# Optimization experiments

Measured on AMD Instinct MI355X. Metric: run time of the kernel, lower is better.

## Reference

```python
import jax, jax.numpy as jnp
import numpy as np

B = 4096
N_DENSE = 13
N_SPARSE = 26
VOCAB = 100000
EMB = 8
CIN_SIZE = [26, 128, 128]


def setup_inputs() -> dict:
    key = jax.random.key(0)
    ks = jax.random.split(key, 24)
    s = 0.05
    dense = jax.random.normal(ks[0], (B, N_DENSE), dtype=jnp.float32)
    sparse = jax.random.randint(ks[1], (B, N_SPARSE), 0, VOCAB).astype(jnp.float32)
    inputs = jnp.concatenate([dense, sparse], axis=1)  # [B, 39]
    emb_tables = jax.random.normal(ks[2], (N_SPARSE, VOCAB, EMB), dtype=jnp.float32) * s
    linear_W = jax.random.normal(ks[3], (39, 1), dtype=jnp.float32) * s
    linear_b = jnp.zeros((1,), dtype=jnp.float32)
    # CIN Conv3d weights: kernel (H_prev, H0, 1) with out_channels H_next -> [H_next, H_prev, H0]
    W_cin0 = jax.random.normal(ks[4], (CIN_SIZE[1], CIN_SIZE[0], CIN_SIZE[0]), dtype=jnp.float32) * s
    b_cin0 = jnp.zeros((CIN_SIZE[1],), dtype=jnp.float32)
    W_cin1 = jax.random.normal(ks[5], (CIN_SIZE[2], CIN_SIZE[1], CIN_SIZE[0]), dtype=jnp.float32) * s
    b_cin1 = jnp.zeros((CIN_SIZE[2],), dtype=jnp.float32)
    cin_lin_W = jax.random.normal(ks[6], (256, 1), dtype=jnp.float32) * s
    cin_lin_b = jnp.zeros((1,), dtype=jnp.float32)
    d_W1 = jax.random.normal(ks[7], (221, 256), dtype=jnp.float32) * s
    d_b1 = jnp.zeros((256,), dtype=jnp.float32)
    d_W2 = jax.random.normal(ks[8], (256, 128), dtype=jnp.float32) * s
    d_b2 = jnp.zeros((128,), dtype=jnp.float32)
    d_W3 = jax.random.normal(ks[9], (128, 64), dtype=jnp.float32) * s
    d_b3 = jnp.zeros((64,), dtype=jnp.float32)
    d_W4 = jax.random.normal(ks[10], (64, 1), dtype=jnp.float32) * s
    d_b4 = jnp.zeros((1,), dtype=jnp.float32)
    return dict(inputs=inputs, emb_tables=emb_tables, linear_W=linear_W, linear_b=linear_b,
                W_cin0=W_cin0, b_cin0=b_cin0, W_cin1=W_cin1, b_cin1=b_cin1,
                cin_lin_W=cin_lin_W, cin_lin_b=cin_lin_b,
                d_W1=d_W1, d_b1=d_b1, d_W2=d_W2, d_b2=d_b2,
                d_W3=d_W3, d_b3=d_b3, d_W4=d_W4, d_b4=d_b4)


def reference(inputs, emb_tables, linear_W, linear_b,
              W_cin0, b_cin0, W_cin1, b_cin1, cin_lin_W, cin_lin_b,
              d_W1, d_b1, d_W2, d_b2, d_W3, d_b3, d_W4, d_b4):
    dense_in = inputs[:, :N_DENSE]                       # [B, 13]
    sparse_idx = inputs[:, N_DENSE:].astype(jnp.int32)   # [B, 26]

    # linear part over the raw inputs
    linear_out = inputs @ linear_W + linear_b            # [B, 1]

    # per-field embedding lookup: tables [F, V, E], idx [B, F] -> emb [B, F, E]
    emb = jax.vmap(lambda t, i: t[i], in_axes=(0, 1), out_axes=1)(emb_tables, sparse_idx)

    # CIN: each layer is an outer product over fields followed by a full-extent
    # Conv3d, i.e. X_{l+1}[b,o,k] = sum_{i,j} X_l[b,i,k] * X_0[b,j,k] * W[o,i,j] + b[o]
    X0 = emb
    Xi = emb
    res = []
    for W, b in ((W_cin0, b_cin0), (W_cin1, b_cin1)):
        Xi = jnp.einsum('bik,bjk,oij->bok', Xi, X0, W) + b[None, :, None]
        res.append(Xi)
    cin_feat = jnp.sum(jnp.concatenate(res, axis=1), axis=-1)  # [B, 256]
    cin_out = jax.nn.relu(cin_feat @ cin_lin_W + cin_lin_b)    # [B, 1]

    # dense MLP over [dense | flattened embeddings]
    h = jnp.concatenate([dense_in, emb.reshape(emb.shape[0], -1)], axis=1)  # [B, 221]
    h = jax.nn.relu(h @ d_W1 + d_b1)
    h = jax.nn.relu(h @ d_W2 + d_b2)
    h = jax.nn.relu(h @ d_W3 + d_b3)
    dense_out = jax.nn.relu(h @ d_W4 + d_b4)                   # [B, 1]

    return jax.nn.sigmoid(linear_out + cin_out + dense_out).reshape(-1)  # [B]
```

## Files before the change

### kernel.cpp

```cpp
#include <hip/hip_runtime.h>
#include <math.h>

#define B     4096
#define ND    13
#define NS    26
#define NF    39
#define VOCAB 100000
#define NP    351
#define NPP   360
#define CHP   45
#define GSTR  28
#define RPB   8
#define TPB   512
#define XSS   212

#define OFF_GST 0
#define OFF_CST 10080
#define OFF_C2J 10088

__global__ __launch_bounds__(256) void k_pre(const float* __restrict__ W0,
                                             const float* __restrict__ W1,
                                             const float* __restrict__ b0,
                                             const float* __restrict__ b1,
                                             const float* __restrict__ clw,
                                             float* __restrict__ Gst,
                                             float* __restrict__ cst,
                                             float* __restrict__ c2j) {
    int blk = blockIdx.x, tid = threadIdx.x;
    if (blk < 26) {
        int j = blk;
        __shared__ float vh[2][128];
        __shared__ float vj[128];
        __shared__ float c2r[2];
        {
            int i = tid & 127, h = tid >> 7;
            const float* wp = W1 + (long)(h * 64) * 3328 + i * 26 + j;
            float acc = 0.f;
#pragma unroll 8
            for (int o = 0; o < 64; o++) acc += clw[128 + h * 64 + o] * wp[o * 3328];
            vh[h][i] = acc;
        }
        __syncthreads();
        if (tid < 128) {
            float vv = vh[0][tid] + vh[1][tid];
            vj[tid] = vv;
            float c = vv * b0[tid];
            for (int off = 32; off; off >>= 1) c += __shfl_down(c, off, 64);
            if ((tid & 63) == 0) c2r[tid >> 6] = c;
        }
        __syncthreads();
        if (tid == 0) c2j[j] = c2r[0] + c2r[1];
        for (int p = tid; p < NPP; p += 256) {
            float g = 0.f;
            if (p < NP) {
                int l = 0, rem = p;
                while (rem >= NS - l) { rem -= NS - l; l++; }
                int m = l + rem;
                float sym = (l != m) ? 1.f : 0.f;
                const float* wa = W0 + l * 26 + m;
                const float* wb = W0 + m * 26 + l;
#pragma unroll 8
                for (int i = 0; i < 128; i++)
                    g += vj[i] * (wa[i * 676] + sym * wb[i * 676]);
            }
            Gst[p * GSTR + j] = g;
        }
    } else if (blk == 26) {
        for (int p = tid; p < NPP; p += 256) {
            float a = 0.f; int lmbits = 0;
            if (p < NP) {
                int l = 0, rem = p;
                while (rem >= NS - l) { rem -= NS - l; l++; }
                int m = l + rem;
                float sym = (l != m) ? 1.f : 0.f;
                const float* wa = W0 + l * 26 + m;
                const float* wb = W0 + m * 26 + l;
#pragma unroll 8
                for (int o = 0; o < 128; o++)
                    a += clw[o] * (wa[o * 676] + sym * wb[o * 676]);
                lmbits = (l << 5) | m;
            }
            Gst[p * GSTR + 26] = a;
            Gst[p * GSTR + 27] = __int_as_float(lmbits);
        }
    } else {
        __shared__ float red[2];
        float c = 0.f;
        if (tid < 128) {
            c = clw[tid] * b0[tid] + clw[128 + tid] * b1[tid];
            for (int off = 32; off; off >>= 1) c += __shfl_down(c, off, 64);
            if ((tid & 63) == 0) red[tid >> 6] = c;
        }
        __syncthreads();
        if (tid == 0) cst[0] = 8.f * (red[0] + red[1]);
    }
}

__global__ __launch_bounds__(512, 4) void k_main(
    const float* __restrict__ inputs, const float* __restrict__ tables,
    const float* __restrict__ lW, const float* __restrict__ lb,
    const float* __restrict__ Gst, const float* __restrict__ c2j,
    const float* __restrict__ cst,
    const float* __restrict__ dW1, const float* __restrict__ db1,
    const float* __restrict__ dW2, const float* __restrict__ db2,
    const float* __restrict__ dW3, const float* __restrict__ db3,
    const float* __restrict__ dW4, const float* __restrict__ db4,
    const float* __restrict__ clb,
    float* __restrict__ out) {
    __shared__ float insf[RPB][40];
    __shared__ float xs[RPB][XSS];
    __shared__ float4 inT4[448];
    __shared__ float h1Tf[256 * 12];
    __shared__ float4 pbuf4[1024];
    __shared__ float lin_s[RPB], scin_s[RPB];
    __shared__ float redbuf[8][RPB];

    float* inTf = (float*)inT4;
    float* h2Tf = (float*)inT4;

    int tid = threadIdx.x;
    int b0r = blockIdx.x * RPB;

    if (tid < RPB * NS) {
        int r = tid / NS, f = tid - r * NS;
        float fidx = inputs[(b0r + r) * NF + ND + f];
        int idx = (int)fidx;
        const float4* src = (const float4*)(tables + ((long)f * VOCAB + idx) * 8);
        float4 a = src[0], b4 = src[1];
        *(float4*)&xs[r][f * 8] = a;
        *(float4*)&xs[r][f * 8 + 4] = b4;
    }
    for (int e = tid; e < RPB * NF; e += TPB) {
        int r = e / NF, c = e - r * NF;
        insf[r][c] = inputs[(b0r + r) * NF + c];
    }
    if (tid >= 496 && tid < 496 + RPB) {
        int r = tid - 496;
        float acc = lb[0];
        for (int c = 0; c < NF; c++) acc += inputs[(b0r + r) * NF + c] * lW[c];
        lin_s[r] = acc;
    }
    __syncthreads();

    for (int e = tid; e < 221 * RPB; e += TPB) {
        int c = e >> 3, r = e & 7;
        inTf[c * 8 + r] = (c < ND) ? insf[r][c] : xs[r][c - ND];
    }
    {
        int w = tid >> 6;
        int wu = __builtin_amdgcn_readfirstlane(w);
        int lane = tid & 63;
        int row = lane >> 3, k = lane & 7;
        const float4* g4 = (const float4*)Gst + wu * CHP * 7;
        const float* xrow = &xs[row][0];
        float csel = (wu == 0) ? 1.f : 0.f;
        float t[27];
#pragma unroll
        for (int j = 0; j < 27; j++) t[j] = 0.f;
#pragma unroll 3
        for (int pi = 0; pi < CHP; pi++) {
            float4 g6 = g4[pi * 7 + 6];
            int lm = __float_as_int(g6.w);
            float q = xrow[(lm >> 5) * 8 + k] * xrow[(lm & 31) * 8 + k];
            float4 g0 = g4[pi * 7 + 0], g1 = g4[pi * 7 + 1];
            float4 g2 = g4[pi * 7 + 2], g3 = g4[pi * 7 + 3];
            float4 g4v = g4[pi * 7 + 4], g5 = g4[pi * 7 + 5];
            t[0]  += g0.x * q; t[1]  += g0.y * q; t[2]  += g0.z * q; t[3]  += g0.w * q;
            t[4]  += g1.x * q; t[5]  += g1.y * q; t[6]  += g1.z * q; t[7]  += g1.w * q;
            t[8]  += g2.x * q; t[9]  += g2.y * q; t[10] += g2.z * q; t[11] += g2.w * q;
            t[12] += g3.x * q; t[13] += g3.y * q; t[14] += g3.z * q; t[15] += g3.w * q;
            t[16] += g4v.x * q; t[17] += g4v.y * q; t[18] += g4v.z * q; t[19] += g4v.w * q;
            t[20] += g5.x * q; t[21] += g5.y * q; t[22] += g5.z * q; t[23] += g5.w * q;
            t[24] += g6.x * q; t[25] += g6.y * q; t[26] += g6.z * q;
        }
        float part = t[26];
#pragma unroll
        for (int j = 0; j < 26; j++) {
            float xv = xrow[j * 8 + k];
            part += (t[j] + csel * c2j[j]) * xv;
        }
        part += __shfl_xor(part, 1, 64);
        part += __shfl_xor(part, 2, 64);
        part += __shfl_xor(part, 4, 64);
        if (k == 0) redbuf[w][row] = part;
    }
    __syncthreads();

    {
        int p = tid & 127, h = (tid >> 7) & 1, cg = tid >> 8;
        int c0 = cg ? 111 : 0;
        int c1 = cg ? 221 : 111;
        float4 A0 = make_float4(0.f, 0.f, 0.f, 0.f);
        float4 A1 = A0;
#pragma unroll 4
        for (int c = c0; c < c1; c++) {
            float2 wv = *(const float2*)&dW1[c * 256 + 2 * p];
            float4 iv = *(const float4*)&inTf[c * 8 + 4 * h];
            A0.x += iv.x * wv.x; A0.y += iv.y * wv.x; A0.z += iv.z * wv.x; A0.w += iv.w * wv.x;
            A1.x += iv.x * wv.y; A1.y += iv.y * wv.y; A1.z += iv.z * wv.y; A1.w += iv.w * wv.y;
        }
        pbuf4[tid * 2]     = A0;
        pbuf4[tid * 2 + 1] = A1;
    }
    __syncthreads();

    if (tid < 256) {
        int o = tid;
        float bb = db1[o];
        float4 a0 = pbuf4[o],       b0v = pbuf4[512 + o];
        float4 a1 = pbuf4[256 + o], b1v = pbuf4[768 + o];
        float4 S0, S1;
        S0.x = fmaxf(a0.x + b0v.x + bb, 0.f); S0.y = fmaxf(a0.y + b0v.y + bb, 0.f);
        S0.z = fmaxf(a0.z + b0v.z + bb, 0.f); S0.w = fmaxf(a0.w + b0v.w + bb, 0.f);
        S1.x = fmaxf(a1.x + b1v.x + bb, 0.f); S1.y = fmaxf(a1.y + b1v.y + bb, 0.f);
        S1.z = fmaxf(a1.z + b1v.z + bb, 0.f); S1.w = fmaxf(a1.w + b1v.w + bb, 0.f);
        *(float4*)&h1Tf[o * 12]     = S0;
        *(float4*)&h1Tf[o * 12 + 4] = S1;
    }
    if (tid >= 256 && tid < 256 + RPB) {
        int r = tid - 256;
        float s = cst[0];
#pragma unroll
        for (int w = 0; w < 8; w++) s += redbuf[w][r];
        scin_s[r] = s;
    }
    __syncthreads();

    {
        int p = tid & 63, h = (tid >> 6) & 1, cg = tid >> 7;
        int c0 = cg << 6;
        float4 A0 = make_float4(0.f, 0.f, 0.f, 0.f);
        float4 A1 = A0;
#pragma unroll 4
        for (int cc = 0; cc < 64; cc++) {
            int c = c0 + cc;
            float2 wv = *(const float2*)&dW2[c * 128 + 2 * p];
            float4 iv = *(const float4*)&h1Tf[c * 12 + 4 * h];
            A0.x += iv.x * wv.x; A0.y += iv.y * wv.x; A0.z += iv.z * wv.x; A0.w += iv.w * wv.x;
            A1.x += iv.x * wv.y; A1.y += iv.y * wv.y; A1.z += iv.z * wv.y; A1.w += iv.w * wv.y;
        }
        pbuf4[tid * 2]     = A0;
        pbuf4[tid * 2 + 1] = A1;
    }
    __syncthreads();

    if (tid < 128) {
        int o = tid;
        float bb = db2[o];
        float sx0 = bb, sy0 = bb, sz0 = bb, sw0 = bb;
        float sx1 = bb, sy1 = bb, sz1 = bb, sw1 = bb;
#pragma unroll
        for (int cg = 0; cg < 4; cg++) {
            float4 p0 = pbuf4[cg * 256 + o];
            float4 p1 = pbuf4[cg * 256 + 128 + o];
            sx0 += p0.x; sy0 += p0.y; sz0 += p0.z; sw0 += p0.w;
            sx1 += p1.x; sy1 += p1.y; sz1 += p1.z; sw1 += p1.w;
        }
        float4 S0, S1;
        S0.x = fmaxf(sx0, 0.f); S0.y = fmaxf(sy0, 0.f);
        S0.z = fmaxf(sz0, 0.f); S0.w = fmaxf(sw0, 0.f);
        S1.x = fmaxf(sx1, 0.f); S1.y = fmaxf(sy1, 0.f);
        S1.z = fmaxf(sz1, 0.f); S1.w = fmaxf(sw1, 0.f);
        *(float4*)&h2Tf[o * 12]     = S0;
        *(float4*)&h2Tf[o * 12 + 4] = S1;
    }
    __syncthreads();

    {
        int cg = tid >> 6, lane = tid & 63;
        int p = lane & 31, h = lane >> 5;
        int c0 = cg << 4;
        float4 A0 = make_float4(0.f, 0.f, 0.f, 0.f);
        float4 A1 = A0;
#pragma unroll 8
        for (int cc = 0; cc < 16; cc++) {
            int c = c0 + cc;
            float2 wv = *(const float2*)&dW3[c * 64 + 2 * p];
            float4 iv = *(const float4*)&h2Tf[c * 12 + 4 * h];
            A0.x += iv.x * wv.x; A0.y += iv.y * wv.x; A0.z += iv.z * wv.x; A0.w += iv.w * wv.x;
            A1.x += iv.x * wv.y; A1.y += iv.y * wv.y; A1.z += iv.z * wv.y; A1.w += iv.w * wv.y;
        }
        pbuf4[tid * 2]     = A0;
        pbuf4[tid * 2 + 1] = A1;
    }
    __syncthreads();

    if (tid < 64) {
        int o = tid;
        float4 S0 = make_float4(0.f, 0.f, 0.f, 0.f);
        float4 S1 = S0;
#pragma unroll
        for (int cg = 0; cg < 8; cg++) {
            float4 p0 = pbuf4[cg * 128 + o];
            float4 p1 = pbuf4[cg * 128 + 64 + o];
            S0.x += p0.x; S0.y += p0.y; S0.z += p0.z; S0.w += p0.w;
            S1.x += p1.x; S1.y += p1.y; S1.z += p1.z; S1.w += p1.w;
        }
        float b3 = db3[o], w4 = dW4[o];
        S0.x = fmaxf(S0.x + b3, 0.f) * w4; S0.y = fmaxf(S0.y + b3, 0.f) * w4;
        S0.z = fmaxf(S0.z + b3, 0.f) * w4; S0.w = fmaxf(S0.w + b3, 0.f) * w4;
        S1.x = fmaxf(S1.x + b3, 0.f) * w4; S1.y = fmaxf(S1.y + b3, 0.f) * w4;
        S1.z = fmaxf(S1.z + b3, 0.f) * w4; S1.w = fmaxf(S1.w + b3, 0.f) * w4;
#pragma unroll
        for (int off = 1; off < 64; off <<= 1) {
            S0.x += __shfl_xor(S0.x, off, 64); S0.y += __shfl_xor(S0.y, off, 64);
            S0.z += __shfl_xor(S0.z, off, 64); S0.w += __shfl_xor(S0.w, off, 64);
            S1.x += __shfl_xor(S1.x, off, 64); S1.y += __shfl_xor(S1.y, off, 64);
            S1.z += __shfl_xor(S1.z, off, 64); S1.w += __shfl_xor(S1.w, off, 64);
        }
        if (tid == 0) {
            float sv[8] = { S0.x, S0.y, S0.z, S0.w, S1.x, S1.y, S1.z, S1.w };
            float bb = db4[0], cb = clb[0];
#pragma unroll
            for (int r = 0; r < RPB; r++) {
                float dense = fmaxf(sv[r] + bb, 0.f);
                float cin = fmaxf(scin_s[r] + cb, 0.f);
                float x = lin_s[r] + cin + dense;
                out[b0r + r] = 1.f / (1.f + expf(-x));
            }
        }
    }
}

extern "C" void kernel_launch(void* const* d_in, const int* in_sizes, int n_in,
                              void* d_out, int out_size, void* d_ws, size_t ws_size,
                              hipStream_t stream) {
    const float* inputs = (const float*)d_in[0];
    const float* tables = (const float*)d_in[1];
    const float* lW     = (const float*)d_in[2];
    const float* lb     = (const float*)d_in[3];
    const float* W0     = (const float*)d_in[4];
    const float* b0     = (const float*)d_in[5];
    const float* W1c    = (const float*)d_in[6];
    const float* b1c    = (const float*)d_in[7];
    const float* clw    = (const float*)d_in[8];
    const float* clb    = (const float*)d_in[9];
    const float* dW1    = (const float*)d_in[10];
    const float* db1    = (const float*)d_in[11];
    const float* dW2    = (const float*)d_in[12];
    const float* db2    = (const float*)d_in[13];
    const float* dW3    = (const float*)d_in[14];
    const float* db3    = (const float*)d_in[15];
    const float* dW4    = (const float*)d_in[16];
    const float* db4    = (const float*)d_in[17];

    float* ws   = (float*)d_ws;
    float* Gst  = ws + OFF_GST;
    float* cst  = ws + OFF_CST;
    float* c2j  = ws + OFF_C2J;

    k_pre<<<28, 256, 0, stream>>>(W0, W1c, b0, b1c, clw, Gst, cst, c2j);
    k_main<<<B / RPB, TPB, 0, stream>>>(inputs, tables, lW, lb, Gst, c2j, cst,
                                        dW1, db1, dW2, db2, dW3, db3, dW4, db4, clb,
                                        (float*)d_out);
}
```

Before: 208.9 us.

## Overlap CIN and first dense layer across warp halves, drop partial reductions

Splits the block so four warps compute the CIN quadratic form, each handling two chunks, while the other four warps compute the full first MLP layer over all 221 inputs without a split-K partial buffer. Other changes: the embedding gather now uses two threads per field, (l,m) index pairs come from a separate LUT, MLP layers 2 and 3 use one output per thread, and the final reduction is spread across all warps. The aim is to remove several barriers and partial-sum passes and to let CIN and dense work run concurrently. The cost is fewer threads per stage and more serial work per thread in each half, which may lengthen the critical path.

```diff
diff --git a/kernel.cpp b/kernel.cpp
--- a/kernel.cpp
+++ b/kernel.cpp
@@ -17,6 +17,7 @@
 #define OFF_GST 0
 #define OFF_CST 10080
 #define OFF_C2J 10088
+#define OFF_LUT 10120
 
 __global__ __launch_bounds__(256) void k_pre(const float* __restrict__ W0,
                                              const float* __restrict__ W1,
@@ -25,7 +26,8 @@
                                              const float* __restrict__ clw,
                                              float* __restrict__ Gst,
                                              float* __restrict__ cst,
-                                             float* __restrict__ c2j) {
+                                             float* __restrict__ c2j,
+                                             int* __restrict__ lutg) {
     int blk = blockIdx.x, tid = threadIdx.x;
     if (blk < 26) {
         int j = blk;
@@ -82,6 +84,7 @@
             }
             Gst[p * GSTR + 26] = a;
             Gst[p * GSTR + 27] = __int_as_float(lmbits);
+            lutg[p] = lmbits;
         }
     } else {
         __shared__ float red[2];
@@ -100,147 +103,130 @@
     const float* __restrict__ inputs, const float* __restrict__ tables,
     const float* __restrict__ lW, const float* __restrict__ lb,
     const float* __restrict__ Gst, const float* __restrict__ c2j,
-    const float* __restrict__ cst,
+    const float* __restrict__ cst, const int* __restrict__ lutg,
     const float* __restrict__ dW1, const float* __restrict__ db1,
     const float* __restrict__ dW2, const float* __restrict__ db2,
     const float* __restrict__ dW3, const float* __restrict__ db3,
     const float* __restrict__ dW4, const float* __restrict__ db4,
     const float* __restrict__ clb,
     float* __restrict__ out) {
-    __shared__ float insf[RPB][40];
     __shared__ float xs[RPB][XSS];
-    __shared__ float4 inT4[448];
+    __shared__ float inTf[221 * 8];
     __shared__ float h1Tf[256 * 12];
     __shared__ float4 pbuf4[1024];
-    __shared__ float lin_s[RPB], scin_s[RPB];
-    __shared__ float redbuf[8][RPB];
-
-    float* inTf = (float*)inT4;
-    float* h2Tf = (float*)inT4;
+    __shared__ float lin_s[RPB];
+    __shared__ float redbuf[4][RPB];
+
+    float* h2Tf = inTf;
+    float* pbufF = (float*)pbuf4;
 
     int tid = threadIdx.x;
     int b0r = blockIdx.x * RPB;
 
-    if (tid < RPB * NS) {
-        int r = tid / NS, f = tid - r * NS;
-        float fidx = inputs[(b0r + r) * NF + ND + f];
-        int idx = (int)fidx;
+    if (tid < 416) {
+        int r = tid / 52, t2 = tid - r * 52;
+        int f = t2 >> 1, hf = t2 & 1;
+        int idx = (int)inputs[(b0r + r) * NF + ND + f];
         const float4* src = (const float4*)(tables + ((long)f * VOCAB + idx) * 8);
-        float4 a = src[0], b4 = src[1];
-        *(float4*)&xs[r][f * 8] = a;
-        *(float4*)&xs[r][f * 8 + 4] = b4;
-    }
-    for (int e = tid; e < RPB * NF; e += TPB) {
-        int r = e / NF, c = e - r * NF;
-        insf[r][c] = inputs[(b0r + r) * NF + c];
-    }
-    if (tid >= 496 && tid < 496 + RPB) {
-        int r = tid - 496;
+        *(float4*)&xs[r][f * 8 + hf * 4] = src[hf];
+    }
+    if (tid >= 448 && tid < 448 + RPB) {
+        int r = tid - 448;
         float acc = lb[0];
         for (int c = 0; c < NF; c++) acc += inputs[(b0r + r) * NF + c] * lW[c];
         lin_s[r] = acc;
     }
     __syncthreads();
 
-    for (int e = tid; e < 221 * RPB; e += TPB) {
+    for (int e = tid; e < 221 * 8; e += TPB) {
         int c = e >> 3, r = e & 7;
-        inTf[c * 8 + r] = (c < ND) ? insf[r][c] : xs[r][c - ND];
-    }
+        inTf[c * 8 + r] = (c < ND) ? inputs[(b0r + r) * NF + c] : xs[r][c - ND];
+    }
+    __syncthreads();
+
     {
         int w = tid >> 6;
         int wu = __builtin_amdgcn_readfirstlane(w);
         int lane = tid & 63;
-        int row = lane >> 3, k = lane & 7;
-        const float4* g4 = (const float4*)Gst + wu * CHP * 7;
-        const float* xrow = &xs[row][0];
-        float csel = (wu == 0) ? 1.f : 0.f;
-        float t[27];
-#pragma unroll
-        for (int j = 0; j < 27; j++) t[j] = 0.f;
-#pragma unroll 3
-        for (int pi = 0; pi < CHP; pi++) {
-            float4 g6 = g4[pi * 7 + 6];
-            int lm = __float_as_int(g6.w);
-            float q = xrow[(lm >> 5) * 8 + k] * xrow[(lm & 31) * 8 + k];
-            float4 g0 = g4[pi * 7 + 0], g1 = g4[pi * 7 + 1];
-            float4 g2 = g4[pi * 7 + 2], g3 = g4[pi * 7 + 3];
-            float4 g4v = g4[pi * 7 + 4], g5 = g4[pi * 7 + 5];
-            t[0]  += g0.x * q; t[1]  += g0.y * q; t[2]  += g0.z * q; t[3]  += g0.w * q;
-            t[4]  += g1.x * q; t[5]  += g1.y * q; t[6]  += g1.z * q; t[7]  += g1.w * q;
-            t[8]  += g2.x * q; t[9]  += g2.y * q; t[10] += g2.z * q; t[11] += g2.w * q;
-            t[12] += g3.x * q; t[13] += g3.y * q; t[14] += g3.z * q; t[15] += g3.w * q;
-            t[16] += g4v.x * q; t[17] += g4v.y * q; t[18] += g4v.z * q; t[19] += g4v.w * q;
-            t[20] += g5.x * q; t[21] += g5.y * q; t[22] += g5.z * q; t[23] += g5.w * q;
-            t[24] += g6.x * q; t[25] += g6.y * q; t[26] += g6.z * q;
-        }
-        float part = t[26];
-#pragma unroll
-        for (int j = 0; j < 26; j++) {
-            float xv = xrow[j * 8 + k];
-            part += (t[j] + csel * c2j[j]) * xv;
-        }
-        part += __shfl_xor(part, 1, 64);
-        part += __shfl_xor(part, 2, 64);
-        part += __shfl_xor(part, 4, 64);
-        if (k == 0) redbuf[w][row] = part;
+        if (wu < 4) {
+            int row = lane >> 3, k = lane & 7;
+            const float* xrow = &xs[row][0];
+            float t[27];
+#pragma unroll
+            for (int j = 0; j < 27; j++) t[j] = 0.f;
+#pragma unroll 1
+            for (int half = 0; half < 2; half++) {
+                int ch = 2 * wu + half;
+                const float4* g4 = (const float4*)Gst + ch * CHP * 7;
+                const int* lu = lutg + ch * CHP;
+#pragma unroll 5
+                for (int pi = 0; pi < CHP; pi++) {
+                    int lm = lu[pi];
+                    float q = xrow[(lm >> 5) * 8 + k] * xrow[(lm & 31) * 8 + k];
+                    float4 g0 = g4[pi * 7 + 0], g1 = g4[pi * 7 + 1];
+                    float4 g2 = g4[pi * 7 + 2], g3 = g4[pi * 7 + 3];
+                    float4 g4v = g4[pi * 7 + 4], g5 = g4[pi * 7 + 5];
+                    float4 g6 = g4[pi * 7 + 6];
+                    t[0]  += g0.x * q; t[1]  += g0.y * q; t[2]  += g0.z * q; t[3]  += g0.w * q;
+                    t[4]  += g1.x * q; t[5]  += g1.y * q; t[6]  += g1.z * q; t[7]  += g1.w * q;
+                    t[8]  += g2.x * q; t[9]  += g2.y * q; t[10] += g2.z * q; t[11] += g2.w * q;
+                    t[12] += g3.x * q; t[13] += g3.y * q; t[14] += g3.z * q; t[15] += g3.w * q;
+                    t[16] += g4v.x * q; t[17] += g4v.y * q; t[18] += g4v.z * q; t[19] += g4v.w * q;
+                    t[20] += g5.x * q; t[21] += g5.y * q; t[22] += g5.z * q; t[23] += g5.w * q;
+                    t[24] += g6.x * q; t[25] += g6.y * q; t[26] += g6.z * q;
+                }
+            }
+            float csel = (wu == 0) ? 1.f : 0.f;
+            float part = t[26];
+#pragma unroll
+            for (int j = 0; j < 26; j++) {
+                float xv = xrow[j * 8 + k];
+                part += (t[j] + csel * c2j[j]) * xv;
+            }
+            part += __shfl_xor(part, 1, 64);
+            part += __shfl_xor(part, 2, 64);
+            part += __shfl_xor(part, 4, 64);
+            if (k == 0) redbuf[wu][row] = part;
+        } else {
+            int o = tid & 255;
+            float4 S0 = make_float4(0.f, 0.f, 0.f, 0.f);
+            float4 S1 = S0;
+#pragma unroll 4
+            for (int c = 0; c < 221; c++) {
+                float wv = dW1[c * 256 + o];
+                float4 i0 = *(const float4*)&inTf[c * 8];
+                float4 i1 = *(const float4*)&inTf[c * 8 + 4];
+                S0.x += i0.x * wv; S0.y += i0.y * wv; S0.z += i0.z * wv; S0.w += i0.w * wv;
+                S1.x += i1.x * wv; S1.y += i1.y * wv; S1.z += i1.z * wv; S1.w += i1.w * wv;
+            }
+            float bb = db1[o];
+            S0.x = fmaxf(S0.x + bb, 0.f); S0.y = fmaxf(S0.y + bb, 0.f);
+            S0.z = fmaxf(S0.z + bb, 0.f); S0.w = fmaxf(S0.w + bb, 0.f);
+            S1.x = fmaxf(S1.x + bb, 0.f); S1.y = fmaxf(S1.y + bb, 0.f);
+            S1.z = fmaxf(S1.z + bb, 0.f); S1.w = fmaxf(S1.w + bb, 0.f);
+            *(float4*)&h1Tf[o * 12]     = S0;
+            *(float4*)&h1Tf[o * 12 + 4] = S1;
+        }
     }
     __syncthreads();
 
     {
-        int p = tid & 127, h = (tid >> 7) & 1, cg = tid >> 8;
-        int c0 = cg ? 111 : 0;
-        int c1 = cg ? 221 : 111;
-        float4 A0 = make_float4(0.f, 0.f, 0.f, 0.f);
-        float4 A1 = A0;
-#pragma unroll 4
-        for (int c = c0; c < c1; c++) {
-            float2 wv = *(const float2*)&dW1[c * 256 + 2 * p];
-            float4 iv = *(const float4*)&inTf[c * 8 + 4 * h];
-            A0.x += iv.x * wv.x; A0.y += iv.y * wv.x; A0.z += iv.z * wv.x; A0.w += iv.w * wv.x;
-            A1.x += iv.x * wv.y; A1.y += iv.y * wv.y; A1.z += iv.z * wv.y; A1.w += iv.w * wv.y;
-        }
-        pbuf4[tid * 2]     = A0;
-        pbuf4[tid * 2 + 1] = A1;
-    }
-    __syncthreads();
-
-    if (tid < 256) {
-        int o = tid;
-        float bb = db1[o];
-        float4 a0 = pbuf4[o],       b0v = pbuf4[512 + o];
-        float4 a1 = pbuf4[256 + o], b1v = pbuf4[768 + o];
-        float4 S0, S1;
-        S0.x = fmaxf(a0.x + b0v.x + bb, 0.f); S0.y = fmaxf(a0.y + b0v.y + bb, 0.f);
-        S0.z = fmaxf(a0.z + b0v.z + bb, 0.f); S0.w = fmaxf(a0.w + b0v.w + bb, 0.f);
-        S1.x = fmaxf(a1.x + b1v.x + bb, 0.f); S1.y = fmaxf(a1.y + b1v.y + bb, 0.f);
-        S1.z = fmaxf(a1.z + b1v.z + bb, 0.f); S1.w = fmaxf(a1.w + b1v.w + bb, 0.f);
-        *(float4*)&h1Tf[o * 12]     = S0;
-        *(float4*)&h1Tf[o * 12 + 4] = S1;
-    }
-    if (tid >= 256 && tid < 256 + RPB) {
-        int r = tid - 256;
-        float s = cst[0];
-#pragma unroll
-        for (int w = 0; w < 8; w++) s += redbuf[w][r];
-        scin_s[r] = s;
-    }
-    __syncthreads();
-
-    {
-        int p = tid & 63, h = (tid >> 6) & 1, cg = tid >> 7;
+        int o = tid & 127, cg = tid >> 7;
         int c0 = cg << 6;
         float4 A0 = make_float4(0.f, 0.f, 0.f, 0.f);
         float4 A1 = A0;
 #pragma unroll 4
         for (int cc = 0; cc < 64; cc++) {
             int c = c0 + cc;
-            float2 wv = *(const float2*)&dW2[c * 128 + 2 * p];
-            float4 iv = *(const float4*)&h1Tf[c * 12 + 4 * h];
-            A0.x += iv.x * wv.x; A0.y += iv.y * wv.x; A0.z += iv.z * wv.x; A0.w += iv.w * wv.x;
-            A1.x += iv.x * wv.y; A1.y += iv.y * wv.y; A1.z += iv.z * wv.y; A1.w += iv.w * wv.y;
-        }
-        pbuf4[tid * 2]     = A0;
-        pbuf4[tid * 2 + 1] = A1;
+            float wv = dW2[c * 128 + o];
+            float4 i0 = *(const float4*)&h1Tf[c * 12];
+            float4 i1 = *(const float4*)&h1Tf[c * 12 + 4];
+            A0.x += i0.x * wv; A0.y += i0.y * wv; A0.z += i0.z * wv; A0.w += i0.w * wv;
+            A1.x += i1.x * wv; A1.y += i1.y * wv; A1.z += i1.z * wv; A1.w += i1.w * wv;
+        }
+        int pb = (cg * 128 + o) * 2;
+        pbuf4[pb]     = A0;
+        pbuf4[pb + 1] = A1;
     }
     __syncthreads();
 
@@ -251,8 +237,8 @@
         float sx1 = bb, sy1 = bb, sz1 = bb, sw1 = bb;
 #pragma unroll
         for (int cg = 0; cg < 4; cg++) {
-            float4 p0 = pbuf4[cg * 256 + o];
-            float4 p1 = pbuf4[cg * 256 + 128 + o];
+            float4 p0 = pbuf4[(cg * 128 + o) * 2];
+            float4 p1 = pbuf4[(cg * 128 + o) * 2 + 1];
             sx0 += p0.x; sy0 += p0.y; sz0 += p0.z; sw0 += p0.w;
             sx1 += p1.x; sy1 += p1.y; sz1 += p1.z; sw1 += p1.w;
         }
@@ -267,57 +253,46 @@
     __syncthreads();
 
     {
-        int cg = tid >> 6, lane = tid & 63;
-        int p = lane & 31, h = lane >> 5;
+        int o = tid & 63, cg = tid >> 6;
         int c0 = cg << 4;
         float4 A0 = make_float4(0.f, 0.f, 0.f, 0.f);
         float4 A1 = A0;
 #pragma unroll 8
         for (int cc = 0; cc < 16; cc++) {
             int c = c0 + cc;
-            float2 wv = *(const float2*)&dW3[c * 64 + 2 * p];
-            float4 iv = *(const float4*)&h2Tf[c * 12 + 4 * h];
-            A0.x += iv.x * wv.x; A0.y += iv.y * wv.x; A0.z += iv.z * wv.x; A0.w += iv.w * wv.x;
-            A1.x += iv.x * wv.y; A1.y += iv.y * wv.y; A1.z += iv.z * wv.y; A1.w += iv.w * wv.y;
-        }
-        pbuf4[tid * 2]     = A0;
-        pbuf4[tid * 2 + 1] = A1;
-    }
-    __syncthreads();
-
-    if (tid < 64) {
-        int o = tid;
-        float4 S0 = make_float4(0.f, 0.f, 0.f, 0.f);
-        float4 S1 = S0;
-#pragma unroll
-        for (int cg = 0; cg < 8; cg++) {
-            float4 p0 = pbuf4[cg * 128 + o];
-            float4 p1 = pbuf4[cg * 128 + 64 + o];
-            S0.x += p0.x; S0.y += p0.y; S0.z += p0.z; S0.w += p0.w;
-            S1.x += p1.x; S1.y += p1.y; S1.z += p1.z; S1.w += p1.w;
-        }
-        float b3 = db3[o], w4 = dW4[o];
-        S0.x = fmaxf(S0.x + b3, 0.f) * w4; S0.y = fmaxf(S0.y + b3, 0.f) * w4;
-        S0.z = fmaxf(S0.z + b3, 0.f) * w4; S0.w = fmaxf(S0.w + b3, 0.f) * w4;
-        S1.x = fmaxf(S1.x + b3, 0.f) * w4; S1.y = fmaxf(S1.y + b3, 0.f) * w4;
-        S1.z = fmaxf(S1.z + b3, 0.f) * w4; S1.w = fmaxf(S1.w + b3, 0.f) * w4;
-#pragma unroll
-        for (int off = 1; off < 64; off <<= 1) {
-            S0.x += __shfl_xor(S0.x, off, 64); S0.y += __shfl_xor(S0.y, off, 64);
-            S0.z += __shfl_xor(S0.z, off, 64); S0.w += __shfl_xor(S0.w, off, 64);
-            S1.x += __shfl_xor(S1.x, off, 64); S1.y += __shfl_xor(S1.y, off, 64);
-            S1.z += __shfl_xor(S1.z, off, 64); S1.w += __shfl_xor(S1.w, off, 64);
-        }
-        if (tid == 0) {
-            float sv[8] = { S0.x, S0.y, S0.z, S0.w, S1.x, S1.y, S1.z, S1.w };
-            float bb = db4[0], cb = clb[0];
-#pragma unroll
-            for (int r = 0; r < RPB; r++) {
-                float dense = fmaxf(sv[r] + bb, 0.f);
-                float cin = fmaxf(scin_s[r] + cb, 0.f);
-                float x = lin_s[r] + cin + dense;
-                out[b0r + r] = 1.f / (1.f + expf(-x));
-            }
+            float wv = dW3[c * 64 + o];
+            float4 i0 = *(const float4*)&h2Tf[c * 12];
+            float4 i1 = *(const float4*)&h2Tf[c * 12 + 4];
+            A0.x += i0.x * wv; A0.y += i0.y * wv; A0.z += i0.z * wv; A0.w += i0.w * wv;
+            A1.x += i1.x * wv; A1.y += i1.y * wv; A1.z += i1.z * wv; A1.w += i1.w * wv;
+        }
+        int pb = (cg * 64 + o) * 2;
+        pbuf4[pb]     = A0;
+        pbuf4[pb + 1] = A1;
+    }
+    __syncthreads();
+
+    {
+        int r = tid >> 6, o = tid & 63;
+        float s = 0.f;
+#pragma unroll
+        for (int cg = 0; cg < 8; cg++)
+            s += pbufF[(cg * 64 + o) * 8 + r];
+        float h3 = fmaxf(s + db3[o], 0.f) * dW4[o];
+        h3 += __shfl_xor(h3, 1, 64);
+        h3 += __shfl_xor(h3, 2, 64);
+        h3 += __shfl_xor(h3, 4, 64);
+        h3 += __shfl_xor(h3, 8, 64);
+        h3 += __shfl_xor(h3, 16, 64);
+        h3 += __shfl_xor(h3, 32, 64);
+        if (o == 0) {
+            float scin = cst[0];
+#pragma unroll
+            for (int w = 0; w < 4; w++) scin += redbuf[w][r];
+            float dense = fmaxf(h3 + db4[0], 0.f);
+            float cin = fmaxf(scin + clb[0], 0.f);
+            float x = lin_s[r] + cin + dense;
+            out[b0r + r] = 1.f / (1.f + expf(-x));
         }
     }
 }
@@ -348,9 +323,10 @@
     float* Gst  = ws + OFF_GST;
     float* cst  = ws + OFF_CST;
     float* c2j  = ws + OFF_C2J;
-
-    k_pre<<<28, 256, 0, stream>>>(W0, W1c, b0, b1c, clw, Gst, cst, c2j);
-    k_main<<<B / RPB, TPB, 0, stream>>>(inputs, tables, lW, lb, Gst, c2j, cst,
+    int*   lutg = (int*)(ws + OFF_LUT);
+
+    k_pre<<<28, 256, 0, stream>>>(W0, W1c, b0, b1c, clw, Gst, cst, c2j, lutg);
+    k_main<<<B / RPB, TPB, 0, stream>>>(inputs, tables, lW, lb, Gst, c2j, cst, lutg,
                                         dW1, db1, dW2, db2, dW3, db3, dW4, db4, clb,
                                         (float*)d_out);
 }
```

New measurement: 222.6 us. +6.6%, slower.
